# Optimization experiments

Measured on AMD Instinct MI355X. Metric: run time of the kernel, lower is better.

Reference implementation:

```python
import jax, jax.numpy as jnp
import numpy as np

GROUP = 8          # weight_group_size
QMAX = 7.0         # 2**(4-1)-1, narrow-range symmetric int4
EPS = 1e-8


def quant_dequant(w):
    """Per-group (size 8, along in_features) symmetric int4 quant-dequant.
    w: [out, in] -> dequantized [out, in]."""
    O, I = w.shape
    wg = w.reshape(O, I // GROUP, GROUP)
    scale = jnp.max(jnp.abs(wg), axis=-1, keepdims=True) / QMAX  # [O, I/G, 1]
    scale = jnp.maximum(scale, EPS)
    q = jnp.clip(jnp.round(wg / scale), -QMAX, QMAX)
    return (q * scale).reshape(O, I)


def setup_inputs() -> dict:
    key = jax.random.key(0)
    kx, kw, kb = jax.random.split(key, 3)
    tokens, din, dout = 8192, 4096, 4096
    x = jax.random.normal(kx, (tokens, din), dtype=jnp.float32)
    weight = jax.random.normal(kw, (dout, din), dtype=jnp.float32) * 0.02
    bias = jax.random.normal(kb, (dout,), dtype=jnp.float32) * 0.01
    return {"x": x, "weight": weight, "bias": bias}


def reference(x, weight, bias):
    w_deq = quant_dequant(weight)                 # [out, in]
    return jnp.dot(x, w_deq.T) + bias             # [tokens, out]
```

## Files before the change

kernel.cpp:

```cpp
#include <hip/hip_runtime.h>
#include <hip/hip_bf16.h>
#include <stdint.h>

typedef __attribute__((ext_vector_type(8))) __bf16 bf16x8;
typedef __attribute__((ext_vector_type(4))) float f32x4;
typedef __attribute__((ext_vector_type(8))) unsigned short ushort8;

typedef const void __attribute__((address_space(1))) gv_t;
typedef void __attribute__((address_space(3))) lv_t;

#define GL16(g, l) __builtin_amdgcn_global_load_lds((gv_t*)(g), (lv_t*)(l), 16, 0, 0)

__device__ __forceinline__ unsigned short f2bf(float f) {
    unsigned int u = __float_as_uint(f);
    u += 0x7fffu + ((u >> 16) & 1u);
    return (unsigned short)(u >> 16);
}

__global__ void __launch_bounds__(256) qdq_weight(const float* __restrict__ w,
                                                  unsigned short* __restrict__ wb,
                                                  int n_groups) {
    int g = blockIdx.x * 256 + threadIdx.x;
    if (g >= n_groups) return;
    const float4* p = (const float4*)w + (size_t)g * 2;
    float4 v0 = p[0], v1 = p[1];
    float t[8] = {v0.x, v0.y, v0.z, v0.w, v1.x, v1.y, v1.z, v1.w};
    float amax = 0.0f;
#pragma unroll
    for (int j = 0; j < 8; ++j) amax = fmaxf(amax, fabsf(t[j]));
    float scale = fmaxf(amax / 7.0f, 1e-8f);
    ushort8 o;
#pragma unroll
    for (int j = 0; j < 8; ++j) {
        float q = rintf(t[j] / scale);
        q = fminf(fmaxf(q, -7.0f), 7.0f);
        o[j] = f2bf(q * scale);
    }
    *((ushort8*)wb + g) = o;
}

__global__ void __launch_bounds__(256) cvt_bf16(const float* __restrict__ x,
                                                unsigned short* __restrict__ xb,
                                                int n8) {
    int i = blockIdx.x * 256 + threadIdx.x;
    if (i >= n8) return;
    const float4* p = (const float4*)x + (size_t)i * 2;
    float4 v0 = p[0], v1 = p[1];
    ushort8 o;
    o[0] = f2bf(v0.x); o[1] = f2bf(v0.y); o[2] = f2bf(v0.z); o[3] = f2bf(v0.w);
    o[4] = f2bf(v1.x); o[5] = f2bf(v1.y); o[6] = f2bf(v1.z); o[7] = f2bf(v1.w);
    *((ushort8*)xb + i) = o;
}

#define BM 256
#define BN 256
#define BK 64

#define MFMA_Q(qm, qn, AF, BF)                                                 \
    __builtin_amdgcn_s_setprio(1);                                             \
    _Pragma("unroll")                                                          \
    for (int mi = 0; mi < 4; ++mi)                                             \
        _Pragma("unroll")                                                      \
        for (int ni = 0; ni < 2; ++ni)                                         \
            _Pragma("unroll")                                                  \
            for (int ks = 0; ks < 2; ++ks)                                     \
                acc[(qm) * 4 + mi][(qn) * 2 + ni] =                            \
                    __builtin_amdgcn_mfma_f32_16x16x32_bf16(                   \
                        AF[mi][ks], BF[ni][ks],                                \
                        acc[(qm) * 4 + mi][(qn) * 2 + ni], 0, 0, 0);           \
    __builtin_amdgcn_s_setprio(0);

#define STAGE_A(b, h, kk)                                                      \
    {                                                                          \
        GL16(gA + (size_t)((h) * 64 + srow) * K + (kk) + schunk,               \
             &sA[b][h][0] + sldso);                                            \
        GL16(gA + (size_t)((h) * 64 + 128 + srow) * K + (kk) + schunk,         \
             &sA[b][h][64 * BK] + sldso);                                      \
    }
#define STAGE_B(b, h, kk)                                                      \
    {                                                                          \
        GL16(gB + (size_t)((h) * 32 + brow) * K + (kk) + schunk,               \
             &sB[b][h][0] + sldso);                                            \
        GL16(gB + (size_t)((h) * 32 + 128 + brow) * K + (kk) + schunk,         \
             &sB[b][h][64 * BK] + sldso);                                      \
    }

#define READ_A(dst, b, h)                                                      \
    _Pragma("unroll")                                                          \
    for (int mi = 0; mi < 4; ++mi) {                                           \
        const int s_ = (wr * 64 + mi * 16 + lr) * BK;                          \
        dst[mi][0] = *(const bf16x8*)&sA[b][h][s_ + e0];                       \
        dst[mi][1] = *(const bf16x8*)&sA[b][h][s_ + e1];                       \
    }
#define READ_B(dst, b, h)                                                      \
    _Pragma("unroll")                                                          \
    for (int ni = 0; ni < 2; ++ni) {                                           \
        const int s_ = (bcol + ni * 16 + lr) * BK;                             \
        dst[ni][0] = *(const bf16x8*)&sB[b][h][s_ + e0];                       \
        dst[ni][1] = *(const bf16x8*)&sB[b][h][s_ + e1];                       \
    }

#define OPEN_BAR()  __builtin_amdgcn_s_barrier()
#define CLOSE_BAR() asm volatile("s_barrier" ::: "memory")
#define VM(n)       asm volatile("s_waitcnt vmcnt(" #n ")" ::: "memory")

__global__ void __launch_bounds__(512, 2)
gemm256(const unsigned short* __restrict__ A,
        const unsigned short* __restrict__ B,
        const float* __restrict__ bias,
        float* __restrict__ C,
        int M, int N, int K) {
    __shared__ unsigned short sA[2][2][128 * BK];
    __shared__ unsigned short sB[2][2][128 * BK];

    const int t  = threadIdx.x;
    const int w  = t >> 6;
    const int ln = t & 63;
    const int lr = ln & 15;
    const int lk = ln >> 4;
    const int wr = w >> 2;
    const int wc = w & 3;
    const int bcol = (wc >> 1) * 64 + (wc & 1) * 32;

    const int nbn = N / BN;
    const int bid = blockIdx.x;
    const int swz = ((int)gridDim.x & 7) ? bid
                  : ((bid & 7) * ((int)gridDim.x >> 3) + (bid >> 3));
    const int m0 = (swz / nbn) * BM;
    const int n0 = (swz % nbn) * BN;

    const unsigned short* gA = A + (size_t)m0 * K;
    const unsigned short* gB = B + (size_t)n0 * K;

    const int srow   = t >> 3;
    const int brow   = (srow & 31) + ((srow >> 5) << 6);
    const int schunk = (((t & 7) ^ (srow & 7)) << 3);
    const int sldso  = (w * 8) * BK;

    const int sw = (lr & 7) << 3;
    const int e0 = (lk * 8) ^ sw;
    const int e1 = (32 + lk * 8) ^ sw;

    f32x4 acc[8][4];
#pragma unroll
    for (int i = 0; i < 8; ++i)
#pragma unroll
        for (int j = 0; j < 4; ++j)
            acc[i][j] = (f32x4)(0.0f);

    const int NT = K / BK;

    STAGE_A(0, 0, 0); STAGE_B(0, 0, 0);
    STAGE_A(0, 1, 0); STAGE_B(0, 1, 0);
    STAGE_A(1, 0, BK); STAGE_B(1, 0, BK);
    VM(4);
    CLOSE_BAR();

    for (int it = 0; it < NT / 2; ++it) {
        const int t0  = 2 * it;
        const int kC  = (t0 + 1) * BK;
        const int kN0 = (t0 + 2) * BK;
        const int kN1 = (t0 + 3) * BK;
        const bool st = (t0 + 2 < NT);

        bf16x8 a0[4][2], a1[4][2], b0[2][2], b1[2][2];

        READ_A(a0, 0, 0); READ_B(b0, 0, 0);
        STAGE_A(1, 1, kC);
        OPEN_BAR();
        MFMA_Q(0, 0, a0, b0);
        CLOSE_BAR();

        READ_A(a1, 0, 1);
        STAGE_B(1, 1, kC);
        OPEN_BAR();
        MFMA_Q(1, 0, a1, b0);
        CLOSE_BAR();

        READ_B(b1, 0, 1);
        if (st) STAGE_A(0, 0, kN0);
        OPEN_BAR();
        MFMA_Q(1, 1, a1, b1);
        CLOSE_BAR();

        if (st) STAGE_B(0, 0, kN0);
        OPEN_BAR();
        MFMA_Q(0, 1, a0, b1);
        if (st) VM(4); else VM(0);
        CLOSE_BAR();

        READ_A(a0, 1, 0); READ_B(b0, 1, 0);
        if (st) STAGE_A(0, 1, kN0);
        OPEN_BAR();
        MFMA_Q(0, 0, a0, b0);
        CLOSE_BAR();

        READ_A(a1, 1, 1);
        if (st) STAGE_B(0, 1, kN0);
        OPEN_BAR();
        MFMA_Q(1, 0, a1, b0);
        CLOSE_BAR();

        READ_B(b1, 1, 1);
        if (st) STAGE_A(1, 0, kN1);
        OPEN_BAR();
        MFMA_Q(1, 1, a1, b1);
        CLOSE_BAR();

        if (st) STAGE_B(1, 0, kN1);
        OPEN_BAR();
        MFMA_Q(0, 1, a0, b1);
        if (st) VM(4); else VM(0);
        CLOSE_BAR();
    }

#pragma unroll
    for (int j = 0; j < 4; ++j) {
        const int n = n0 + wc * 64 + (j >> 1) * 32 + (j & 1) * 16 + lr;
        const float bv = bias[n];
#pragma unroll
        for (int i = 0; i < 8; ++i) {
            const int m = m0 + wr * 128 + (i >> 2) * 64 + (i & 3) * 16 + lk * 4;
            f32x4 v = acc[i][j];
            C[(size_t)(m + 0) * N + n] = v[0] + bv;
            C[(size_t)(m + 1) * N + n] = v[1] + bv;
            C[(size_t)(m + 2) * N + n] = v[2] + bv;
            C[(size_t)(m + 3) * N + n] = v[3] + bv;
        }
    }
}

extern "C" void kernel_launch(void* const* d_in, const int* in_sizes, int n_in,
                              void* d_out, int out_size, void* d_ws, size_t ws_size,
                              hipStream_t stream) {
    const float* x    = (const float*)d_in[0];
    const float* wgt  = (const float*)d_in[1];
    const float* bias = (const float*)d_in[2];
    float* out        = (float*)d_out;

    const int dout = in_sizes[2];
    const int din  = in_sizes[1] / dout;
    const int M    = in_sizes[0] / din;
    const int N    = dout, K = din;

    unsigned short* xb = (unsigned short*)d_ws;
    unsigned short* wb = xb + (size_t)M * K;

    const int ng_w = (N * K) / 8;
    qdq_weight<<<(ng_w + 255) / 256, 256, 0, stream>>>(wgt, wb, ng_w);

    const int n8_x = (M * K) / 8;
    cvt_bf16<<<(n8_x + 255) / 256, 256, 0, stream>>>(x, xb, n8_x);

    const int nwg = (M / BM) * (N / BN);
    gemm256<<<nwg, 512, 0, stream>>>(xb, wb, bias, out, M, N, K);
}
```

Measured before the change: 306.8 us.

## Restructure GEMM main loop into deeper prefetch pipeline with one barrier per phase

After: 307.8 us. About the same (+0.3%).

```diff
diff --git a/kernel.cpp b/kernel.cpp
--- a/kernel.cpp
+++ b/kernel.cpp
@@ -100,9 +100,8 @@
         dst[ni][1] = *(const bf16x8*)&sB[b][h][s_ + e1];                       \
     }
 
-#define OPEN_BAR()  __builtin_amdgcn_s_barrier()
-#define CLOSE_BAR() asm volatile("s_barrier" ::: "memory")
-#define VM(n)       asm volatile("s_waitcnt vmcnt(" #n ")" ::: "memory")
+#define BAR()  asm volatile("s_barrier" ::: "memory")
+#define VM(n)  asm volatile("s_waitcnt vmcnt(" #n ")" ::: "memory")
 
 __global__ void __launch_bounds__(512, 2)
 gemm256(const unsigned short* __restrict__ A,
@@ -149,69 +148,64 @@
             acc[i][j] = (f32x4)(0.0f);
 
     const int NT = K / BK;
-
-    STAGE_A(0, 0, 0); STAGE_B(0, 0, 0);
-    STAGE_A(0, 1, 0); STAGE_B(0, 1, 0);
-    STAGE_A(1, 0, BK); STAGE_B(1, 0, BK);
-    VM(4);
-    CLOSE_BAR();
-
-    for (int it = 0; it < NT / 2; ++it) {
-        const int t0  = 2 * it;
-        const int kC  = (t0 + 1) * BK;
-        const int kN0 = (t0 + 2) * BK;
-        const int kN1 = (t0 + 3) * BK;
-        const bool st = (t0 + 2 < NT);
-
-        bf16x8 a0[4][2], a1[4][2], b0[2][2], b1[2][2];
-
-        READ_A(a0, 0, 0); READ_B(b0, 0, 0);
-        STAGE_A(1, 1, kC);
-        OPEN_BAR();
-        MFMA_Q(0, 0, a0, b0);
-        CLOSE_BAR();
-
-        READ_A(a1, 0, 1);
-        STAGE_B(1, 1, kC);
-        OPEN_BAR();
-        MFMA_Q(1, 0, a1, b0);
-        CLOSE_BAR();
-
-        READ_B(b1, 0, 1);
-        if (st) STAGE_A(0, 0, kN0);
-        OPEN_BAR();
-        MFMA_Q(1, 1, a1, b1);
-        CLOSE_BAR();
-
-        if (st) STAGE_B(0, 0, kN0);
-        OPEN_BAR();
-        MFMA_Q(0, 1, a0, b1);
-        if (st) VM(4); else VM(0);
-        CLOSE_BAR();
-
-        READ_A(a0, 1, 0); READ_B(b0, 1, 0);
-        if (st) STAGE_A(0, 1, kN0);
-        OPEN_BAR();
-        MFMA_Q(0, 0, a0, b0);
-        CLOSE_BAR();
-
-        READ_A(a1, 1, 1);
-        if (st) STAGE_B(0, 1, kN0);
-        OPEN_BAR();
-        MFMA_Q(1, 0, a1, b0);
-        CLOSE_BAR();
-
-        READ_B(b1, 1, 1);
-        if (st) STAGE_A(1, 0, kN1);
-        OPEN_BAR();
-        MFMA_Q(1, 1, a1, b1);
-        CLOSE_BAR();
-
-        if (st) STAGE_B(1, 0, kN1);
-        OPEN_BAR();
-        MFMA_Q(0, 1, a0, b1);
-        if (st) VM(4); else VM(0);
-        CLOSE_BAR();
+    const int J  = NT / 2;
+
+    bf16x8 a0f[4][2], a1f[4][2], b0f[2][2], b1f[2][2];
+
+    STAGE_A(0, 0, 0);
+    STAGE_B(0, 0, 0);
+    STAGE_B(0, 1, 0);
+    STAGE_A(0, 1, 0);
+    STAGE_A(1, 0, BK);
+    STAGE_B(1, 0, BK);
+    STAGE_B(1, 1, BK);
+    VM(8);
+    BAR();
+    READ_A(a0f, 0, 0);
+
+    for (int it = 0; it < J; ++it) {
+        const int t0 = 2 * it;
+        const int k1 = (t0 + 1) * BK;
+        int k2 = (t0 + 2) * BK;  if (k2 >= K) k2 = 0;
+        int k3 = (t0 + 3) * BK;  if (k3 >= K) k3 = 0;
+
+        READ_B(b0f, 0, 0); READ_B(b1f, 0, 1);
+        STAGE_A(1, 1, k1);
+        MFMA_Q(0, 0, a0f, b0f);
+        VM(8); BAR();
+
+        READ_A(a1f, 0, 1);
+        STAGE_A(0, 0, k2);
+        MFMA_Q(0, 1, a0f, b1f);
+        VM(8); BAR();
+
+        READ_A(a0f, 1, 0);
+        STAGE_B(0, 0, k2);
+        MFMA_Q(1, 1, a1f, b1f);
+        VM(8); BAR();
+
+        STAGE_B(0, 1, k2);
+        MFMA_Q(1, 0, a1f, b0f);
+        VM(8); BAR();
+
+        READ_B(b0f, 1, 0); READ_B(b1f, 1, 1);
+        STAGE_A(0, 1, k2);
+        MFMA_Q(0, 0, a0f, b0f);
+        VM(8); BAR();
+
+        READ_A(a1f, 1, 1);
+        STAGE_A(1, 0, k3);
+        MFMA_Q(0, 1, a0f, b1f);
+        VM(8); BAR();
+
+        READ_A(a0f, 0, 0);
+        STAGE_B(1, 0, k3);
+        MFMA_Q(1, 1, a1f, b1f);
+        VM(8); BAR();
+
+        STAGE_B(1, 1, k3);
+        MFMA_Q(1, 0, a1f, b0f);
+        VM(8); BAR();
     }
 
 #pragma unroll
```
